# Kernel tuning notes

Measured on AMD Instinct MI355X. Metric: run time of the kernel, lower is better.

## Reference

```python
import jax, jax.numpy as jnp
import numpy as np

D_MODEL = 512
NUM_HEADS = 8
D_K = D_MODEL // NUM_HEADS


def setup_inputs() -> dict:
    key = jax.random.key(0)
    ks = jax.random.split(key, 9)
    s = 1.0 / np.sqrt(D_MODEL)
    x = jax.random.normal(ks[0], (2, 4096, D_MODEL), dtype=jnp.float32)
    Wq = jax.random.uniform(ks[1], (D_MODEL, D_MODEL), jnp.float32, -s, s)
    bq = jax.random.uniform(ks[2], (D_MODEL,), jnp.float32, -s, s)
    Wk = jax.random.uniform(ks[3], (D_MODEL, D_MODEL), jnp.float32, -s, s)
    bk = jax.random.uniform(ks[4], (D_MODEL,), jnp.float32, -s, s)
    Wv = jax.random.uniform(ks[5], (D_MODEL, D_MODEL), jnp.float32, -s, s)
    bv = jax.random.uniform(ks[6], (D_MODEL,), jnp.float32, -s, s)
    Wo = jax.random.uniform(ks[7], (D_MODEL, D_MODEL), jnp.float32, -s, s)
    bo = jax.random.uniform(ks[8], (D_MODEL,), jnp.float32, -s, s)
    return {"x": x, "Wq": Wq, "bq": bq, "Wk": Wk, "bk": bk,
            "Wv": Wv, "bv": bv, "Wo": Wo, "bo": bo}


def reference(x, Wq, bq, Wk, bk, Wv, bv, Wo, bo):
    B, S, _ = x.shape
    # projections; split heads -> [B, H, S, d_k]
    def heads(t):
        return t.reshape(B, S, NUM_HEADS, D_K).transpose(0, 2, 1, 3)
    Q = heads(x @ Wq + bq)
    K = heads(x @ Wk + bk)
    V = heads(x @ Wv + bv)
    scores = jnp.einsum('bhqd,bhkd->bhqk', Q, K) / jnp.sqrt(jnp.float32(D_K))
    attn = jax.nn.softmax(scores, axis=-1)
    out = jnp.einsum('bhqk,bhkd->bhqd', attn, V)
    out = out.transpose(0, 2, 1, 3).reshape(B, S, D_MODEL)
    return out @ Wo + bo
```

## Files before the change

kernel.cpp:

```cpp
#include <hip/hip_runtime.h>
#include <hip/hip_bf16.h>

#define S_LEN 4096
#define DMODEL 512
#define NHEADS 8
#define DK 64
#define BATCH 2
#define MROWS (BATCH * S_LEN)

typedef __attribute__((ext_vector_type(8))) short bf16x8;
typedef __attribute__((ext_vector_type(4))) float f32x4;
typedef unsigned short ushort_t;

__device__ __forceinline__ unsigned packbf(float a, float b) {
  unsigned r;
  asm("v_cvt_pk_bf16_f32 %0, %1, %2" : "=v"(r) : "v"(a), "v"(b));
  return r;
}

__device__ __forceinline__ unsigned short bf1(float a) {
  union { __hip_bfloat16 h; unsigned short s; } u;
  u.h = __float2bfloat16(a);
  return u.s;
}

__device__ __forceinline__ float bflo(unsigned u) { return __uint_as_float(u << 16); }
__device__ __forceinline__ float bfhi(unsigned u) { return __uint_as_float(u & 0xFFFF0000u); }

__device__ __forceinline__ float fastrcp(float x) {
  float r;
  asm("v_rcp_f32 %0, %1" : "=v"(r) : "v"(x));
  return r;
}

__device__ __forceinline__ void gll16(const void* g, void* l) {
  __builtin_amdgcn_global_load_lds(
      (const __attribute__((address_space(1))) unsigned*)g,
      (__attribute__((address_space(3))) unsigned*)l, 16, 0, 0);
}

__global__ __launch_bounds__(256) void prep(
    const float* __restrict__ x, const float* __restrict__ Wq,
    const float* __restrict__ Wk, const float* __restrict__ Wv,
    const float* __restrict__ Wo, ushort_t* __restrict__ xbf,
    ushort_t* __restrict__ Wcat, ushort_t* __restrict__ Wot) {
  __shared__ float T[32][33];
  const int bid = blockIdx.x;
  const int tid = threadIdx.x;
  if (bid < 2048) {
    size_t i = ((size_t)bid * 256 + tid) * 8;
    float4 a = *reinterpret_cast<const float4*>(x + i);
    float4 b = *reinterpret_cast<const float4*>(x + i + 4);
    uint4 o;
    o.x = packbf(a.x, a.y);
    o.y = packbf(a.z, a.w);
    o.z = packbf(b.x, b.y);
    o.w = packbf(b.z, b.w);
    *reinterpret_cast<uint4*>(xbf + i) = o;
  } else {
    int t = bid - 2048;
    int w = t >> 8;
    int tile = t & 255;
    int k0 = (tile & 15) * 32, n0 = (tile >> 4) * 32;
    const float* W = w == 0 ? Wq : (w == 1 ? Wk : (w == 2 ? Wv : Wo));
    ushort_t* out = (w == 3) ? Wot : (Wcat + (size_t)w * 512 * 512);
    const int r = tid >> 3, c4 = (tid & 7) * 4;
    float4 v = *reinterpret_cast<const float4*>(W + (size_t)(k0 + r) * 512 + n0 + c4);
    T[r][c4 + 0] = v.x; T[r][c4 + 1] = v.y; T[r][c4 + 2] = v.z; T[r][c4 + 3] = v.w;
    __syncthreads();
    uint2 o;
    o.x = packbf(T[c4 + 0][r], T[c4 + 1][r]);
    o.y = packbf(T[c4 + 2][r], T[c4 + 3][r]);
    *reinterpret_cast<uint2*>(out + (size_t)(n0 + r) * 512 + k0 + c4) = o;
  }
}

__global__ __launch_bounds__(256) void gemm_qkv(
    const ushort_t* __restrict__ A, const ushort_t* __restrict__ Wcat,
    const float* __restrict__ bq, const float* __restrict__ bk,
    const float* __restrict__ bv, ushort_t* __restrict__ Qo,
    ushort_t* __restrict__ Ko, ushort_t* __restrict__ Vo, float CQ) {
  __shared__ ushort_t AL[2][128 * 32];
  __shared__ ushort_t BL[2][128 * 32];
  const int tid = threadIdx.x;
  const int wid = tid >> 6;
  const int lane = tid & 63;
  const int ql = lane & 15;
  const int g = lane >> 4;
  const int wr = wid >> 1, wc = wid & 1;

  const int p = blockIdx.x;
  const int xcd = p & 7, q_ = p >> 3;
  const int mi = xcd * 8 + q_ / 12;
  const int ni = q_ % 12;
  const int m0 = mi * 128, n0 = ni * 128;
  const int region = n0 >> 9;

  f32x4 acc[4][4];
#pragma unroll
  for (int i = 0; i < 4; ++i)
#pragma unroll
    for (int j = 0; j < 4; ++j) acc[i][j] = (f32x4){0.f, 0.f, 0.f, 0.f};

  auto stage = [&](int k0, int buf) {
#pragma unroll
    for (int i = 0; i < 2; ++i) {
      int idx = i * 256 + tid;
      int r = idx >> 2;
      int c = (idx & 3) * 8;
      gll16(A + (size_t)(m0 + r) * 512 + k0 + c, &AL[buf][idx * 8]);
      gll16(Wcat + (size_t)(n0 + r) * 512 + k0 + c, &BL[buf][idx * 8]);
    }
  };

  stage(0, 0);
  __syncthreads();
  int buf = 0;

  for (int t = 0; t < 16; ++t) {
    if (t < 15) stage((t + 1) * 32, buf ^ 1);
    const ushort_t* ALb = &AL[buf][0];
    const ushort_t* BLb = &BL[buf][0];
    bf16x8 af[4], bfr[4];
#pragma unroll
    for (int mi2 = 0; mi2 < 4; ++mi2)
      af[mi2] = *reinterpret_cast<const bf16x8*>(ALb + (wr * 64 + mi2 * 16 + ql) * 32 + g * 8);
#pragma unroll
    for (int ni2 = 0; ni2 < 4; ++ni2)
      bfr[ni2] = *reinterpret_cast<const bf16x8*>(BLb + (wc * 64 + ni2 * 16 + ql) * 32 + g * 8);
#pragma unroll
    for (int mi2 = 0; mi2 < 4; ++mi2)
#pragma unroll
      for (int ni2 = 0; ni2 < 4; ++ni2)
        acc[mi2][ni2] = __builtin_amdgcn_mfma_f32_16x16x32_bf16(af[mi2], bfr[ni2], acc[mi2][ni2], 0, 0, 0);
    __syncthreads();
    buf ^= 1;
  }

  const float* bias = region == 0 ? bq : (region == 1 ? bk : bv);
  const float scale = region == 0 ? CQ : 1.0f;
  const int nl0 = n0 - (region << 9);
  ushort_t* outT = region == 0 ? Qo : Ko;

  float bvv[4];
#pragma unroll
  for (int ni2 = 0; ni2 < 4; ++ni2) bvv[ni2] = bias[nl0 + wc * 64 + ni2 * 16 + ql];

#pragma unroll
  for (int mi2 = 0; mi2 < 4; ++mi2) {
#pragma unroll
    for (int ni2 = 0; ni2 < 4; ++ni2) {
      int nl = nl0 + wc * 64 + ni2 * 16 + ql;
      int h = nl >> 6, d = nl & 63;
#pragma unroll
      for (int reg = 0; reg < 4; ++reg) {
        float val = (acc[mi2][ni2][reg] + bvv[ni2]) * scale;
        int m = m0 + wr * 64 + mi2 * 16 + 4 * g + reg;
        int b = m >> 12, s = m & 4095;
        if (region <= 1) {
          outT[(((size_t)(b * NHEADS + h) * S_LEN + s) * DK) + d] = bf1(val);
        } else {
          int k6 = s & 63;
          int pos = (k6 & 32) | (((k6 >> 2) & 3) << 3) | (((k6 >> 4) & 1) << 2) | (k6 & 3);
          int sperm = (s & ~63) | pos;
          Vo[(((size_t)(b * NHEADS + h) * DK + d) * S_LEN) + sperm] = bf1(val);
        }
      }
    }
  }
}

__global__ __launch_bounds__(256) void gemm_wo_fused(
    const ushort_t* __restrict__ Opart, const float* __restrict__ Lpart,
    const ushort_t* __restrict__ Wt, const float* __restrict__ bias,
    float* __restrict__ out) {
  __shared__ ushort_t AL[2][128 * 32];
  __shared__ ushort_t BL[2][128 * 32];
  const int tid = threadIdx.x;
  const int wid = tid >> 6;
  const int lane = tid & 63;
  const int ql = lane & 15;
  const int g = lane >> 4;
  const int wr = wid >> 1, wc = wid & 1;

  const int p = blockIdx.x;
  const int L = (p & 7) * 32 + (p >> 3);
  const int m0 = (L >> 2) * 128, n0 = (L & 3) * 128;

  f32x4 acc[4][4];
#pragma unroll
  for (int i = 0; i < 4; ++i)
#pragma unroll
    for (int j = 0; j < 4; ++j) acc[i][j] = (f32x4){0.f, 0.f, 0.f, 0.f};

  const int r_[2] = {tid >> 2, 256 / 4 + (tid >> 2)};
  const int c8 = (tid & 3) * 8;

  int sA[2], bhbase[2];
#pragma unroll
  for (int i = 0; i < 2; ++i) {
    int m = m0 + r_[i];
    int b = m >> 12;
    sA[i] = m & 4095;
    bhbase[i] = b * 8;
  }

  auto loadA = [&](int k0, uint4 av[2], float inv[2]) {
    int kg = k0 + c8;
    int h = kg >> 6, d = kg & 63;
#pragma unroll
    for (int i = 0; i < 2; ++i) {
      int bh = bhbase[i] + h;
      size_t off = ((size_t)bh * S_LEN + sA[i]) * 64 + d;
      av[i] = *reinterpret_cast<const uint4*>(Opart + off);
      uint4 a1 = *reinterpret_cast<const uint4*>(Opart + off + (size_t)16 * S_LEN * 64);
      float l = Lpart[(size_t)bh * S_LEN + sA[i]] + Lpart[((size_t)(16 + bh)) * S_LEN + sA[i]];
      inv[i] = fastrcp(l);
      unsigned u0[4] = {av[i].x, av[i].y, av[i].z, av[i].w};
      unsigned u1[4] = {a1.x, a1.y, a1.z, a1.w};
      unsigned r[4];
#pragma unroll
      for (int j = 0; j < 4; ++j) {
        float e0 = (bflo(u0[j]) + bflo(u1[j])) * inv[i];
        float e1 = (bfhi(u0[j]) + bfhi(u1[j])) * inv[i];
        r[j] = packbf(e0, e1);
      }
      av[i].x = r[0]; av[i].y = r[1]; av[i].z = r[2]; av[i].w = r[3];
    }
  };

  auto writeA = [&](int buf, uint4 av[2]) {
#pragma unroll
    for (int i = 0; i < 2; ++i) {
      int idx = i * 256 + tid;
      *reinterpret_cast<uint4*>(&AL[buf][idx * 8]) = av[i];
    }
  };

  auto stageB = [&](int k0, int buf) {
#pragma unroll
    for (int i = 0; i < 2; ++i) {
      int idx = i * 256 + tid;
      int r = idx >> 2;
      int c = (idx & 3) * 8;
      gll16(Wt + (size_t)(n0 + r) * 512 + k0 + c, &BL[buf][idx * 8]);
    }
  };

  {
    uint4 av[2]; float inv[2];
    loadA(0, av, inv);
    writeA(0, av);
    stageB(0, 0);
  }
  __syncthreads();

  for (int t = 0; t < 16; ++t) {
    const int buf = t & 1;
    uint4 av[2]; float inv[2];
    if (t < 15) {
      stageB((t + 1) * 32, buf ^ 1);
      loadA((t + 1) * 32, av, inv);
    }
    const ushort_t* ALb = &AL[buf][0];
    const ushort_t* BLb = &BL[buf][0];
    bf16x8 af[4], bfr[4];
#pragma unroll
    for (int mi = 0; mi < 4; ++mi)
      af[mi] = *reinterpret_cast<const bf16x8*>(ALb + (wr * 64 + mi * 16 + ql) * 32 + g * 8);
#pragma unroll
    for (int ni = 0; ni < 4; ++ni)
      bfr[ni] = *reinterpret_cast<const bf16x8*>(BLb + (wc * 64 + ni * 16 + ql) * 32 + g * 8);
#pragma unroll
    for (int mi = 0; mi < 4; ++mi)
#pragma unroll
      for (int ni = 0; ni < 4; ++ni)
        acc[mi][ni] = __builtin_amdgcn_mfma_f32_16x16x32_bf16(af[mi], bfr[ni], acc[mi][ni], 0, 0, 0);
    if (t < 15) writeA(buf ^ 1, av);
    __syncthreads();
  }

  float bv[4];
#pragma unroll
  for (int ni = 0; ni < 4; ++ni) bv[ni] = bias[n0 + wc * 64 + ni * 16 + ql];

#pragma unroll
  for (int mi = 0; mi < 4; ++mi) {
#pragma unroll
    for (int ni = 0; ni < 4; ++ni) {
      int n = n0 + wc * 64 + ni * 16 + ql;
#pragma unroll
      for (int reg = 0; reg < 4; ++reg) {
        int m = m0 + wr * 64 + mi * 16 + 4 * g + reg;
        out[(size_t)m * 512 + n] = acc[mi][ni][reg] + bv[ni];
      }
    }
  }
}

__global__ __launch_bounds__(256) void gemm_wo(
    const ushort_t* __restrict__ A, const ushort_t* __restrict__ Wt,
    const float* __restrict__ bias, float* __restrict__ out) {
  __shared__ ushort_t AL[2][128 * 32];
  __shared__ ushort_t BL[2][128 * 32];
  const int tid = threadIdx.x;
  const int wid = tid >> 6;
  const int lane = tid & 63;
  const int ql = lane & 15;
  const int g = lane >> 4;
  const int wr = wid >> 1, wc = wid & 1;
  const int m0 = blockIdx.x * 128, n0 = blockIdx.y * 128;

  f32x4 acc[4][4];
#pragma unroll
  for (int i = 0; i < 4; ++i)
#pragma unroll
    for (int j = 0; j < 4; ++j) acc[i][j] = (f32x4){0.f, 0.f, 0.f, 0.f};

  auto stage = [&](int k0, int buf) {
#pragma unroll
    for (int i = 0; i < 2; ++i) {
      int idx = i * 256 + tid;
      int r = idx >> 2;
      int c = (idx & 3) * 8;
      gll16(A + (size_t)(m0 + r) * 512 + k0 + c, &AL[buf][idx * 8]);
      gll16(Wt + (size_t)(n0 + r) * 512 + k0 + c, &BL[buf][idx * 8]);
    }
  };

  stage(0, 0);
  __syncthreads();
  int buf = 0;

  for (int t = 0; t < 16; ++t) {
    if (t < 15) stage((t + 1) * 32, buf ^ 1);
    const ushort_t* ALb = &AL[buf][0];
    const ushort_t* BLb = &BL[buf][0];
    bf16x8 af[4], bfr[4];
#pragma unroll
    for (int mi = 0; mi < 4; ++mi)
      af[mi] = *reinterpret_cast<const bf16x8*>(ALb + (wr * 64 + mi * 16 + ql) * 32 + g * 8);
#pragma unroll
    for (int ni = 0; ni < 4; ++ni)
      bfr[ni] = *reinterpret_cast<const bf16x8*>(BLb + (wc * 64 + ni * 16 + ql) * 32 + g * 8);
#pragma unroll
    for (int mi = 0; mi < 4; ++mi)
#pragma unroll
      for (int ni = 0; ni < 4; ++ni)
        acc[mi][ni] = __builtin_amdgcn_mfma_f32_16x16x32_bf16(af[mi], bfr[ni], acc[mi][ni], 0, 0, 0);
    __syncthreads();
    buf ^= 1;
  }

  float bv[4];
#pragma unroll
  for (int ni = 0; ni < 4; ++ni) bv[ni] = bias[n0 + wc * 64 + ni * 16 + ql];

#pragma unroll
  for (int mi = 0; mi < 4; ++mi) {
#pragma unroll
    for (int ni = 0; ni < 4; ++ni) {
      int n = n0 + wc * 64 + ni * 16 + ql;
#pragma unroll
      for (int reg = 0; reg < 4; ++reg) {
        int m = m0 + wr * 64 + mi * 16 + 4 * g + reg;
        out[(size_t)m * 512 + n] = acc[mi][ni][reg] + bv[ni];
      }
    }
  }
}

template <bool SPLIT2>
__global__ __launch_bounds__(256, 4) void attn_mfma(
    const ushort_t* __restrict__ Q, const ushort_t* __restrict__ K,
    const ushort_t* __restrict__ Vt, ushort_t* __restrict__ AO,
    ushort_t* __restrict__ Opart, float* __restrict__ Lpart) {
  __shared__ ushort_t KL[2][64 * 64];
  __shared__ ushort_t VL[2][64 * 64];

  const int tid = threadIdx.x;
  const int wid = tid >> 6;
  const int lane = tid & 63;
  const int g = lane >> 4;
  const int ql = lane & 15;

  int L;
  if (SPLIT2) {
    int orig = blockIdx.x;
    L = (orig & 7) * 128 + (orig >> 3);
  } else {
    L = blockIdx.x;
  }
  const int qt = L & 31;
  const int bhsp = L >> 5;
  const int sp = SPLIT2 ? (bhsp & 1) : 0;
  const int bh = SPLIT2 ? (bhsp >> 1) : bhsp;
  const int NT = SPLIT2 ? 32 : 64;
  const int t0 = sp * NT;

  const ushort_t* Qb = Q + (size_t)bh * S_LEN * DK;
  const ushort_t* Kb = K + (size_t)bh * S_LEN * DK;
  const ushort_t* Vb = Vt + (size_t)bh * DK * S_LEN;

  const int qbase = qt * 128 + wid * 32;

  bf16x8 qf[2][2];
#pragma unroll
  for (int c = 0; c < 2; ++c) {
    int q = qbase + c * 16 + ql;
#pragma unroll
    for (int t = 0; t < 2; ++t)
      qf[c][t] = *reinterpret_cast<const bf16x8*>(Qb + (size_t)q * DK + t * 32 + g * 8);
  }

  bf16x8 ones;
#pragma unroll
  for (int j = 0; j < 8; ++j) ones[j] = (short)0x3F80;

  f32x4 ot[4][2];
#pragma unroll
  for (int db = 0; db < 4; ++db)
#pragma unroll
    for (int c = 0; c < 2; ++c) ot[db][c] = (f32x4){0.f, 0.f, 0.f, 0.f};
  f32x4 lacc[2];
  lacc[0] = (f32x4){0.f, 0.f, 0.f, 0.f};
  lacc[1] = (f32x4){0.f, 0.f, 0.f, 0.f};

  const int srow = lane >> 3;
  const int schk = lane & 7;
  const int r0 = wid * 16 + srow;
  const int r1 = r0 + 8;
  const int ssc = (schk ^ srow) << 4;

  const char* gk0 = (const char*)Kb + ((size_t)(t0 * 64 + r0)) * 128 + ssc;
  const char* gk1 = (const char*)Kb + ((size_t)(t0 * 64 + r1)) * 128 + ssc;
  const char* gv0 = (const char*)Vb + (size_t)r0 * (S_LEN * 2) + (size_t)t0 * 128 + ssc;
  const char* gv1 = (const char*)Vb + (size_t)r1 * (S_LEN * 2) + (size_t)t0 * 128 + ssc;

  char* lkA0 = (char*)&KL[0][0] + (wid * 16) * 128 + lane * 16;
  char* lkB0 = lkA0 + 8 * 128;
  char* lkA1 = lkA0 + 8192;
  char* lkB1 = lkB0 + 8192;
  char* lvA0 = (char*)&VL[0][0] + (wid * 16) * 128 + lane * 16;
  char* lvB0 = lvA0 + 8 * 128;
  char* lvA1 = lvA0 + 8192;
  char* lvB1 = lvB0 + 8192;

  int koA[4], koB[4];
#pragma unroll
  for (int kb = 0; kb < 4; ++kb) {
    int r = kb * 16 + ql;
    koA[kb] = r * 128 + (((g) ^ (r & 7)) << 4);
    koB[kb] = r * 128 + (((g + 4) ^ (r & 7)) << 4);
  }
  int voP[2][4];
#pragma unroll
  for (int t = 0; t < 2; ++t)
#pragma unroll
    for (int db = 0; db < 4; ++db) {
      int rd = db * 16 + ql;
      voP[t][db] = rd * 128 + (((t * 4 + g) ^ (rd & 7)) << 4);
    }

  gll16(gk0, lkA0); gll16(gk1, lkB0);
  gll16(gv0, lvA0); gll16(gv1, lvB0);
  gk0 += 8192; gk1 += 8192; gv0 += 128; gv1 += 128;
  __syncthreads();

  auto body = [&](const char* KB, const char* VB, char* dkA, char* dkB,
                  char* dvA, char* dvB, bool pref) {
    if (pref) {
      gll16(gk0, dkA); gll16(gk1, dkB);
      gll16(gv0, dvA); gll16(gv1, dvB);
      gk0 += 8192; gk1 += 8192; gv0 += 128; gv1 += 128;
    }

    f32x4 st[4][2];
    __builtin_amdgcn_s_setprio(1);
#pragma unroll
    for (int kb = 0; kb < 4; ++kb) {
      bf16x8 k0 = *reinterpret_cast<const bf16x8*>(KB + koA[kb]);
      bf16x8 k1 = *reinterpret_cast<const bf16x8*>(KB + koB[kb]);
#pragma unroll
      for (int c = 0; c < 2; ++c) {
        f32x4 z = (f32x4){0.f, 0.f, 0.f, 0.f};
        z = __builtin_amdgcn_mfma_f32_16x16x32_bf16(k0, qf[c][0], z, 0, 0, 0);
        z = __builtin_amdgcn_mfma_f32_16x16x32_bf16(k1, qf[c][1], z, 0, 0, 0);
        st[kb][c] = z;
      }
    }
    __builtin_amdgcn_s_setprio(0);

    unsigned pk[2][4][2];
#pragma unroll
    for (int c = 0; c < 2; ++c)
#pragma unroll
      for (int kb = 0; kb < 4; ++kb)
#pragma unroll
        for (int r2 = 0; r2 < 2; ++r2) {
          float pa = __builtin_amdgcn_exp2f(st[kb][c][2 * r2]);
          float pb_ = __builtin_amdgcn_exp2f(st[kb][c][2 * r2 + 1]);
          pk[c][kb][r2] = packbf(pa, pb_);
        }

    __builtin_amdgcn_s_setprio(1);
#pragma unroll
    for (int t = 0; t < 2; ++t) {
      union { unsigned u[4]; bf16x8 v; } pb0, pb1;
      pb0.u[0] = pk[0][2 * t][0];     pb0.u[1] = pk[0][2 * t][1];
      pb0.u[2] = pk[0][2 * t + 1][0]; pb0.u[3] = pk[0][2 * t + 1][1];
      pb1.u[0] = pk[1][2 * t][0];     pb1.u[1] = pk[1][2 * t][1];
      pb1.u[2] = pk[1][2 * t + 1][0]; pb1.u[3] = pk[1][2 * t + 1][1];
#pragma unroll
      for (int db = 0; db < 4; ++db) {
        bf16x8 af = *reinterpret_cast<const bf16x8*>(VB + voP[t][db]);
        ot[db][0] = __builtin_amdgcn_mfma_f32_16x16x32_bf16(af, pb0.v, ot[db][0], 0, 0, 0);
        ot[db][1] = __builtin_amdgcn_mfma_f32_16x16x32_bf16(af, pb1.v, ot[db][1], 0, 0, 0);
      }
      lacc[0] = __builtin_amdgcn_mfma_f32_16x16x32_bf16(ones, pb0.v, lacc[0], 0, 0, 0);
      lacc[1] = __builtin_amdgcn_mfma_f32_16x16x32_bf16(ones, pb1.v, lacc[1], 0, 0, 0);
    }
    __builtin_amdgcn_s_setprio(0);

    __syncthreads();
  };

  const char* KB0 = (const char*)&KL[0][0];
  const char* VB0 = (const char*)&VL[0][0];
  const char* KB1 = (const char*)&KL[1][0];
  const char* VB1 = (const char*)&VL[1][0];

  for (int it = 0; it < NT; it += 2) {
    body(KB0, VB0, lkA1, lkB1, lvA1, lvB1, true);
    body(KB1, VB1, lkA0, lkB0, lvA0, lvB0, it + 2 < NT);
  }

  if (SPLIT2) {
    ushort_t* Ob = Opart + (((size_t)sp * 16 + bh) * S_LEN) * 64;
#pragma unroll
    for (int c = 0; c < 2; ++c) {
      const int q = qbase + c * 16 + ql;
#pragma unroll
      for (int db = 0; db < 4; ++db) {
        uint2 o;
        o.x = packbf(ot[db][c][0], ot[db][c][1]);
        o.y = packbf(ot[db][c][2], ot[db][c][3]);
        *reinterpret_cast<uint2*>(Ob + (size_t)q * 64 + db * 16 + 4 * g) = o;
      }
      if (g == 0) Lpart[((size_t)sp * 16 + bh) * S_LEN + q] = lacc[c][0];
    }
  } else {
    const int b = bh >> 3, h = bh & 7;
#pragma unroll
    for (int c = 0; c < 2; ++c) {
      const int q = qbase + c * 16 + ql;
      float inv = 1.f / lacc[c][0];
#pragma unroll
      for (int db = 0; db < 4; ++db) {
        uint2 o;
        o.x = packbf(ot[db][c][0] * inv, ot[db][c][1] * inv);
        o.y = packbf(ot[db][c][2] * inv, ot[db][c][3] * inv);
        *reinterpret_cast<uint2*>(AO + ((size_t)b * S_LEN + q) * DMODEL + h * DK + db * 16 + g * 4) = o;
      }
    }
  }
}

extern "C" void kernel_launch(void* const* d_in, const int* in_sizes, int n_in,
                              void* d_out, int out_size, void* d_ws, size_t ws_size,
                              hipStream_t stream) {
  const float* x  = (const float*)d_in[0];
  const float* Wq = (const float*)d_in[1];
  const float* bq = (const float*)d_in[2];
  const float* Wk = (const float*)d_in[3];
  const float* bk = (const float*)d_in[4];
  const float* Wv = (const float*)d_in[5];
  const float* bv = (const float*)d_in[6];
  const float* Wo = (const float*)d_in[7];
  const float* bo = (const float*)d_in[8];
  float* out = (float*)d_out;

  const float CQ = 0.18033688f;

  char* ws = (char*)d_ws;
  const size_t NBF = (size_t)MROWS * DMODEL;
  ushort_t* xbf = (ushort_t*)ws;
  ushort_t* Qbf = (ushort_t*)(ws + NBF * 2);
  ushort_t* Kbf = (ushort_t*)(ws + NBF * 4);
  ushort_t* Vtb = (ushort_t*)(ws + NBF * 6);

  const size_t OFF_WT    = NBF * 8;
  const size_t OFF_LPART = OFF_WT + 4 * 512 * 512 * 2;
  const size_t OFF_OPART = OFF_LPART + 512 * 1024;
  const size_t NEED_SPLIT = OFF_OPART + (size_t)2 * 16 * S_LEN * 64 * 2;
  const bool use_split = ws_size >= NEED_SPLIT;

  ushort_t* Wcat;
  ushort_t* AOb;
  if (use_split) {
    Wcat = (ushort_t*)(ws + OFF_WT);
    AOb = xbf;
  } else {
    AOb = (ushort_t*)(ws + NBF * 8);
    Wcat = (ushort_t*)(ws + NBF * 10);
  }
  ushort_t* Wot = Wcat + 3 * 512 * 512;
  float* Lpart = (float*)(ws + OFF_LPART);
  ushort_t* Opart = (ushort_t*)(ws + OFF_OPART);

  prep<<<3072, 256, 0, stream>>>(x, Wq, Wk, Wv, Wo, xbf, Wcat, Wot);

  gemm_qkv<<<768, 256, 0, stream>>>(xbf, Wcat, bq, bk, bv, Qbf, Kbf, Vtb, CQ);

  if (use_split) {
    attn_mfma<true><<<1024, 256, 0, stream>>>(Qbf, Kbf, Vtb, AOb, Opart, Lpart);
    gemm_wo_fused<<<256, 256, 0, stream>>>(Opart, Lpart, Wot, bo, out);
  } else {
    attn_mfma<false><<<512, 256, 0, stream>>>(Qbf, Kbf, Vtb, AOb, Opart, Lpart);
    dim3 gg(MROWS / 128, DMODEL / 128);
    gemm_wo<<<gg, 256, 0, stream>>>(AOb, Wot, bo, out);
  }
}
```

Baseline: 122.4 us.

## Fuse x bf16 conversion into QKV GEMM, enlarge attention blocks, halve Wo tile

Result: faster. 117.1 us (-4.3%).

```diff
diff --git a/kernel.cpp b/kernel.cpp
--- a/kernel.cpp
+++ b/kernel.cpp
@@ -40,43 +40,29 @@
 }
 
 __global__ __launch_bounds__(256) void prep(
-    const float* __restrict__ x, const float* __restrict__ Wq,
-    const float* __restrict__ Wk, const float* __restrict__ Wv,
-    const float* __restrict__ Wo, ushort_t* __restrict__ xbf,
+    const float* __restrict__ Wq, const float* __restrict__ Wk,
+    const float* __restrict__ Wv, const float* __restrict__ Wo,
     ushort_t* __restrict__ Wcat, ushort_t* __restrict__ Wot) {
   __shared__ float T[32][33];
   const int bid = blockIdx.x;
   const int tid = threadIdx.x;
-  if (bid < 2048) {
-    size_t i = ((size_t)bid * 256 + tid) * 8;
-    float4 a = *reinterpret_cast<const float4*>(x + i);
-    float4 b = *reinterpret_cast<const float4*>(x + i + 4);
-    uint4 o;
-    o.x = packbf(a.x, a.y);
-    o.y = packbf(a.z, a.w);
-    o.z = packbf(b.x, b.y);
-    o.w = packbf(b.z, b.w);
-    *reinterpret_cast<uint4*>(xbf + i) = o;
-  } else {
-    int t = bid - 2048;
-    int w = t >> 8;
-    int tile = t & 255;
-    int k0 = (tile & 15) * 32, n0 = (tile >> 4) * 32;
-    const float* W = w == 0 ? Wq : (w == 1 ? Wk : (w == 2 ? Wv : Wo));
-    ushort_t* out = (w == 3) ? Wot : (Wcat + (size_t)w * 512 * 512);
-    const int r = tid >> 3, c4 = (tid & 7) * 4;
-    float4 v = *reinterpret_cast<const float4*>(W + (size_t)(k0 + r) * 512 + n0 + c4);
-    T[r][c4 + 0] = v.x; T[r][c4 + 1] = v.y; T[r][c4 + 2] = v.z; T[r][c4 + 3] = v.w;
-    __syncthreads();
-    uint2 o;
-    o.x = packbf(T[c4 + 0][r], T[c4 + 1][r]);
-    o.y = packbf(T[c4 + 2][r], T[c4 + 3][r]);
-    *reinterpret_cast<uint2*>(out + (size_t)(n0 + r) * 512 + k0 + c4) = o;
-  }
+  int w = bid >> 8;
+  int tile = bid & 255;
+  int k0 = (tile & 15) * 32, n0 = (tile >> 4) * 32;
+  const float* W = w == 0 ? Wq : (w == 1 ? Wk : (w == 2 ? Wv : Wo));
+  ushort_t* out = (w == 3) ? Wot : (Wcat + (size_t)w * 512 * 512);
+  const int r = tid >> 3, c4 = (tid & 7) * 4;
+  float4 v = *reinterpret_cast<const float4*>(W + (size_t)(k0 + r) * 512 + n0 + c4);
+  T[r][c4 + 0] = v.x; T[r][c4 + 1] = v.y; T[r][c4 + 2] = v.z; T[r][c4 + 3] = v.w;
+  __syncthreads();
+  uint2 o;
+  o.x = packbf(T[c4 + 0][r], T[c4 + 1][r]);
+  o.y = packbf(T[c4 + 2][r], T[c4 + 3][r]);
+  *reinterpret_cast<uint2*>(out + (size_t)(n0 + r) * 512 + k0 + c4) = o;
 }
 
 __global__ __launch_bounds__(256) void gemm_qkv(
-    const ushort_t* __restrict__ A, const ushort_t* __restrict__ Wcat,
+    const float* __restrict__ x, const ushort_t* __restrict__ Wcat,
     const float* __restrict__ bq, const float* __restrict__ bk,
     const float* __restrict__ bv, ushort_t* __restrict__ Qo,
     ushort_t* __restrict__ Ko, ushort_t* __restrict__ Vo, float CQ) {
@@ -102,23 +88,53 @@
 #pragma unroll
     for (int j = 0; j < 4; ++j) acc[i][j] = (f32x4){0.f, 0.f, 0.f, 0.f};
 
-  auto stage = [&](int k0, int buf) {
+  auto loadA = [&](int k0, uint4 av[2]) {
 #pragma unroll
     for (int i = 0; i < 2; ++i) {
       int idx = i * 256 + tid;
       int r = idx >> 2;
       int c = (idx & 3) * 8;
-      gll16(A + (size_t)(m0 + r) * 512 + k0 + c, &AL[buf][idx * 8]);
+      const float* src = x + (size_t)(m0 + r) * 512 + k0 + c;
+      float4 a = *reinterpret_cast<const float4*>(src);
+      float4 b = *reinterpret_cast<const float4*>(src + 4);
+      av[i].x = packbf(a.x, a.y);
+      av[i].y = packbf(a.z, a.w);
+      av[i].z = packbf(b.x, b.y);
+      av[i].w = packbf(b.z, b.w);
+    }
+  };
+  auto writeA = [&](int buf, uint4 av[2]) {
+#pragma unroll
+    for (int i = 0; i < 2; ++i) {
+      int idx = i * 256 + tid;
+      *reinterpret_cast<uint4*>(&AL[buf][idx * 8]) = av[i];
+    }
+  };
+  auto stageB = [&](int k0, int buf) {
+#pragma unroll
+    for (int i = 0; i < 2; ++i) {
+      int idx = i * 256 + tid;
+      int r = idx >> 2;
+      int c = (idx & 3) * 8;
       gll16(Wcat + (size_t)(n0 + r) * 512 + k0 + c, &BL[buf][idx * 8]);
     }
   };
 
-  stage(0, 0);
+  {
+    uint4 av[2];
+    loadA(0, av);
+    writeA(0, av);
+    stageB(0, 0);
+  }
   __syncthreads();
-  int buf = 0;
 
   for (int t = 0; t < 16; ++t) {
-    if (t < 15) stage((t + 1) * 32, buf ^ 1);
+    const int buf = t & 1;
+    uint4 av[2];
+    if (t < 15) {
+      stageB((t + 1) * 32, buf ^ 1);
+      loadA((t + 1) * 32, av);
+    }
     const ushort_t* ALb = &AL[buf][0];
     const ushort_t* BLb = &BL[buf][0];
     bf16x8 af[4], bfr[4];
@@ -133,8 +149,8 @@
 #pragma unroll
       for (int ni2 = 0; ni2 < 4; ++ni2)
         acc[mi2][ni2] = __builtin_amdgcn_mfma_f32_16x16x32_bf16(af[mi2], bfr[ni2], acc[mi2][ni2], 0, 0, 0);
+    if (t < 15) writeA(buf ^ 1, av);
     __syncthreads();
-    buf ^= 1;
   }
 
   const float* bias = region == 0 ? bq : (region == 1 ? bk : bv);
@@ -174,7 +190,7 @@
     const ushort_t* __restrict__ Opart, const float* __restrict__ Lpart,
     const ushort_t* __restrict__ Wt, const float* __restrict__ bias,
     float* __restrict__ out) {
-  __shared__ ushort_t AL[2][128 * 32];
+  __shared__ ushort_t AL[2][64 * 32];
   __shared__ ushort_t BL[2][128 * 32];
   const int tid = threadIdx.x;
   const int wid = tid >> 6;
@@ -184,59 +200,45 @@
   const int wr = wid >> 1, wc = wid & 1;
 
   const int p = blockIdx.x;
-  const int L = (p & 7) * 32 + (p >> 3);
-  const int m0 = (L >> 2) * 128, n0 = (L & 3) * 128;
-
-  f32x4 acc[4][4];
-#pragma unroll
-  for (int i = 0; i < 4; ++i)
+  const int L = (p & 7) * 64 + (p >> 3);
+  const int m0 = (L >> 2) * 64, n0 = (L & 3) * 128;
+
+  f32x4 acc[2][4];
+#pragma unroll
+  for (int i = 0; i < 2; ++i)
 #pragma unroll
     for (int j = 0; j < 4; ++j) acc[i][j] = (f32x4){0.f, 0.f, 0.f, 0.f};
 
-  const int r_[2] = {tid >> 2, 256 / 4 + (tid >> 2)};
+  const int rA = tid >> 2;
   const int c8 = (tid & 3) * 8;
-
-  int sA[2], bhbase[2];
-#pragma unroll
-  for (int i = 0; i < 2; ++i) {
-    int m = m0 + r_[i];
-    int b = m >> 12;
-    sA[i] = m & 4095;
-    bhbase[i] = b * 8;
-  }
-
-  auto loadA = [&](int k0, uint4 av[2], float inv[2]) {
+  const int mrow = m0 + rA;
+  const int bb = mrow >> 12;
+  const int sA = mrow & 4095;
+  const int bhbase = bb * 8;
+
+  auto loadA = [&](int k0, uint4& av) {
     int kg = k0 + c8;
     int h = kg >> 6, d = kg & 63;
-#pragma unroll
-    for (int i = 0; i < 2; ++i) {
-      int bh = bhbase[i] + h;
-      size_t off = ((size_t)bh * S_LEN + sA[i]) * 64 + d;
-      av[i] = *reinterpret_cast<const uint4*>(Opart + off);
-      uint4 a1 = *reinterpret_cast<const uint4*>(Opart + off + (size_t)16 * S_LEN * 64);
-      float l = Lpart[(size_t)bh * S_LEN + sA[i]] + Lpart[((size_t)(16 + bh)) * S_LEN + sA[i]];
-      inv[i] = fastrcp(l);
-      unsigned u0[4] = {av[i].x, av[i].y, av[i].z, av[i].w};
-      unsigned u1[4] = {a1.x, a1.y, a1.z, a1.w};
-      unsigned r[4];
-#pragma unroll
-      for (int j = 0; j < 4; ++j) {
-        float e0 = (bflo(u0[j]) + bflo(u1[j])) * inv[i];
-        float e1 = (bfhi(u0[j]) + bfhi(u1[j])) * inv[i];
-        r[j] = packbf(e0, e1);
-      }
-      av[i].x = r[0]; av[i].y = r[1]; av[i].z = r[2]; av[i].w = r[3];
-    }
-  };
-
-  auto writeA = [&](int buf, uint4 av[2]) {
-#pragma unroll
-    for (int i = 0; i < 2; ++i) {
-      int idx = i * 256 + tid;
-      *reinterpret_cast<uint4*>(&AL[buf][idx * 8]) = av[i];
-    }
-  };
-
+    int bh = bhbase + h;
+    size_t off = ((size_t)bh * S_LEN + sA) * 64 + d;
+    uint4 a0 = *reinterpret_cast<const uint4*>(Opart + off);
+    uint4 a1 = *reinterpret_cast<const uint4*>(Opart + off + (size_t)16 * S_LEN * 64);
+    float l = Lpart[(size_t)bh * S_LEN + sA] + Lpart[(size_t)(16 + bh) * S_LEN + sA];
+    float inv = fastrcp(l);
+    unsigned u0[4] = {a0.x, a0.y, a0.z, a0.w};
+    unsigned u1[4] = {a1.x, a1.y, a1.z, a1.w};
+    unsigned r[4];
+#pragma unroll
+    for (int j = 0; j < 4; ++j) {
+      float e0 = (bflo(u0[j]) + bflo(u1[j])) * inv;
+      float e1 = (bfhi(u0[j]) + bfhi(u1[j])) * inv;
+      r[j] = packbf(e0, e1);
+    }
+    av.x = r[0]; av.y = r[1]; av.z = r[2]; av.w = r[3];
+  };
+  auto writeA = [&](int buf, uint4 av) {
+    *reinterpret_cast<uint4*>(&AL[buf][tid * 8]) = av;
+  };
   auto stageB = [&](int k0, int buf) {
 #pragma unroll
     for (int i = 0; i < 2; ++i) {
@@ -248,8 +250,8 @@
   };
 
   {
-    uint4 av[2]; float inv[2];
-    loadA(0, av, inv);
+    uint4 av;
+    loadA(0, av);
     writeA(0, av);
     stageB(0, 0);
   }
@@ -257,22 +259,22 @@
 
   for (int t = 0; t < 16; ++t) {
     const int buf = t & 1;
-    uint4 av[2]; float inv[2];
+    uint4 av;
     if (t < 15) {
       stageB((t + 1) * 32, buf ^ 1);
-      loadA((t + 1) * 32, av, inv);
+      loadA((t + 1) * 32, av);
     }
     const ushort_t* ALb = &AL[buf][0];
     const ushort_t* BLb = &BL[buf][0];
-    bf16x8 af[4], bfr[4];
-#pragma unroll
-    for (int mi = 0; mi < 4; ++mi)
-      af[mi] = *reinterpret_cast<const bf16x8*>(ALb + (wr * 64 + mi * 16 + ql) * 32 + g * 8);
+    bf16x8 af[2], bfr[4];
+#pragma unroll
+    for (int mi = 0; mi < 2; ++mi)
+      af[mi] = *reinterpret_cast<const bf16x8*>(ALb + (wr * 32 + mi * 16 + ql) * 32 + g * 8);
 #pragma unroll
     for (int ni = 0; ni < 4; ++ni)
       bfr[ni] = *reinterpret_cast<const bf16x8*>(BLb + (wc * 64 + ni * 16 + ql) * 32 + g * 8);
 #pragma unroll
-    for (int mi = 0; mi < 4; ++mi)
+    for (int mi = 0; mi < 2; ++mi)
 #pragma unroll
       for (int ni = 0; ni < 4; ++ni)
         acc[mi][ni] = __builtin_amdgcn_mfma_f32_16x16x32_bf16(af[mi], bfr[ni], acc[mi][ni], 0, 0, 0);
@@ -285,13 +287,13 @@
   for (int ni = 0; ni < 4; ++ni) bv[ni] = bias[n0 + wc * 64 + ni * 16 + ql];
 
 #pragma unroll
-  for (int mi = 0; mi < 4; ++mi) {
+  for (int mi = 0; mi < 2; ++mi) {
 #pragma unroll
     for (int ni = 0; ni < 4; ++ni) {
       int n = n0 + wc * 64 + ni * 16 + ql;
 #pragma unroll
       for (int reg = 0; reg < 4; ++reg) {
-        int m = m0 + wr * 64 + mi * 16 + 4 * g + reg;
+        int m = m0 + wr * 32 + mi * 16 + 4 * g + reg;
         out[(size_t)m * 512 + n] = acc[mi][ni][reg] + bv[ni];
       }
     }
@@ -371,7 +373,7 @@
 }
 
 template <bool SPLIT2>
-__global__ __launch_bounds__(256, 4) void attn_mfma(
+__global__ __launch_bounds__(512, 2) void attn_mfma(
     const ushort_t* __restrict__ Q, const ushort_t* __restrict__ K,
     const ushort_t* __restrict__ Vt, ushort_t* __restrict__ AO,
     ushort_t* __restrict__ Opart, float* __restrict__ Lpart) {
@@ -387,12 +389,12 @@
   int L;
   if (SPLIT2) {
     int orig = blockIdx.x;
-    L = (orig & 7) * 128 + (orig >> 3);
+    L = (orig & 7) * 64 + (orig >> 3);
   } else {
     L = blockIdx.x;
   }
-  const int qt = L & 31;
-  const int bhsp = L >> 5;
+  const int qt = L & 15;
+  const int bhsp = L >> 4;
   const int sp = SPLIT2 ? (bhsp & 1) : 0;
   const int bh = SPLIT2 ? (bhsp >> 1) : bhsp;
   const int NT = SPLIT2 ? 32 : 64;
@@ -402,7 +404,7 @@
   const ushort_t* Kb = K + (size_t)bh * S_LEN * DK;
   const ushort_t* Vb = Vt + (size_t)bh * DK * S_LEN;
 
-  const int qbase = qt * 128 + wid * 32;
+  const int qbase = qt * 256 + wid * 32;
 
   bf16x8 qf[2][2];
 #pragma unroll
@@ -428,23 +430,16 @@
 
   const int srow = lane >> 3;
   const int schk = lane & 7;
-  const int r0 = wid * 16 + srow;
-  const int r1 = r0 + 8;
+  const int r0 = wid * 8 + srow;
   const int ssc = (schk ^ srow) << 4;
 
   const char* gk0 = (const char*)Kb + ((size_t)(t0 * 64 + r0)) * 128 + ssc;
-  const char* gk1 = (const char*)Kb + ((size_t)(t0 * 64 + r1)) * 128 + ssc;
   const char* gv0 = (const char*)Vb + (size_t)r0 * (S_LEN * 2) + (size_t)t0 * 128 + ssc;
-  const char* gv1 = (const char*)Vb + (size_t)r1 * (S_LEN * 2) + (size_t)t0 * 128 + ssc;
-
-  char* lkA0 = (char*)&KL[0][0] + (wid * 16) * 128 + lane * 16;
-  char* lkB0 = lkA0 + 8 * 128;
+
+  char* lkA0 = (char*)&KL[0][0] + (wid * 8) * 128 + lane * 16;
   char* lkA1 = lkA0 + 8192;
-  char* lkB1 = lkB0 + 8192;
-  char* lvA0 = (char*)&VL[0][0] + (wid * 16) * 128 + lane * 16;
-  char* lvB0 = lvA0 + 8 * 128;
+  char* lvA0 = (char*)&VL[0][0] + (wid * 8) * 128 + lane * 16;
   char* lvA1 = lvA0 + 8192;
-  char* lvB1 = lvB0 + 8192;
 
   int koA[4], koB[4];
 #pragma unroll
@@ -462,17 +457,16 @@
       voP[t][db] = rd * 128 + (((t * 4 + g) ^ (rd & 7)) << 4);
     }
 
-  gll16(gk0, lkA0); gll16(gk1, lkB0);
-  gll16(gv0, lvA0); gll16(gv1, lvB0);
-  gk0 += 8192; gk1 += 8192; gv0 += 128; gv1 += 128;
+  gll16(gk0, lkA0);
+  gll16(gv0, lvA0);
+  gk0 += 8192; gv0 += 128;
   __syncthreads();
 
-  auto body = [&](const char* KB, const char* VB, char* dkA, char* dkB,
-                  char* dvA, char* dvB, bool pref) {
+  auto body = [&](const char* KB, const char* VB, char* dkA, char* dvA, bool pref) {
     if (pref) {
-      gll16(gk0, dkA); gll16(gk1, dkB);
-      gll16(gv0, dvA); gll16(gv1, dvB);
-      gk0 += 8192; gk1 += 8192; gv0 += 128; gv1 += 128;
+      gll16(gk0, dkA);
+      gll16(gv0, dvA);
+      gk0 += 8192; gv0 += 128;
     }
 
     f32x4 st[4][2];
@@ -531,8 +525,8 @@
   const char* VB1 = (const char*)&VL[1][0];
 
   for (int it = 0; it < NT; it += 2) {
-    body(KB0, VB0, lkA1, lkB1, lvA1, lvB1, true);
-    body(KB1, VB1, lkA0, lkB0, lvA0, lvB0, it + 2 < NT);
+    body(KB0, VB0, lkA1, lvA1, true);
+    body(KB1, VB1, lkA0, lvA0, it + 2 < NT);
   }
 
   if (SPLIT2) {
@@ -584,7 +578,7 @@
 
   char* ws = (char*)d_ws;
   const size_t NBF = (size_t)MROWS * DMODEL;
-  ushort_t* xbf = (ushort_t*)ws;
+  ushort_t* AObuf = (ushort_t*)ws;
   ushort_t* Qbf = (ushort_t*)(ws + NBF * 2);
   ushort_t* Kbf = (ushort_t*)(ws + NBF * 4);
   ushort_t* Vtb = (ushort_t*)(ws + NBF * 6);
@@ -596,28 +590,25 @@
   const bool use_split = ws_size >= NEED_SPLIT;
 
   ushort_t* Wcat;
-  ushort_t* AOb;
   if (use_split) {
     Wcat = (ushort_t*)(ws + OFF_WT);
-    AOb = xbf;
   } else {
-    AOb = (ushort_t*)(ws + NBF * 8);
     Wcat = (ushort_t*)(ws + NBF * 10);
   }
   ushort_t* Wot = Wcat + 3 * 512 * 512;
   float* Lpart = (float*)(ws + OFF_LPART);
   ushort_t* Opart = (ushort_t*)(ws + OFF_OPART);
 
-  prep<<<3072, 256, 0, stream>>>(x, Wq, Wk, Wv, Wo, xbf, Wcat, Wot);
-
-  gemm_qkv<<<768, 256, 0, stream>>>(xbf, Wcat, bq, bk, bv, Qbf, Kbf, Vtb, CQ);
+  prep<<<1024, 256, 0, stream>>>(Wq, Wk, Wv, Wo, Wcat, Wot);
+
+  gemm_qkv<<<768, 256, 0, stream>>>(x, Wcat, bq, bk, bv, Qbf, Kbf, Vtb, CQ);
 
   if (use_split) {
-    attn_mfma<true><<<1024, 256, 0, stream>>>(Qbf, Kbf, Vtb, AOb, Opart, Lpart);
-    gemm_wo_fused<<<256, 256, 0, stream>>>(Opart, Lpart, Wot, bo, out);
+    attn_mfma<true><<<512, 512, 0, stream>>>(Qbf, Kbf, Vtb, AObuf, Opart, Lpart);
+    gemm_wo_fused<<<512, 256, 0, stream>>>(Opart, Lpart, Wot, bo, out);
   } else {
-    attn_mfma<false><<<512, 256, 0, stream>>>(Qbf, Kbf, Vtb, AOb, Opart, Lpart);
+    attn_mfma<false><<<256, 512, 0, stream>>>(Qbf, Kbf, Vtb, AObuf, Opart, Lpart);
     dim3 gg(MROWS / 128, DMODEL / 128);
-    gemm_wo<<<gg, 256, 0, stream>>>(AOb, Wot, bo, out);
-  }
-}
+    gemm_wo<<<gg, 256, 0, stream>>>(AObuf, Wot, bo, out);
+  }
+}
```
